# Optimization experiments

Hardware: AMD Instinct MI355X
Metric: run time of the kernel (lower is better)

The kernel has to match this reference:

```python
import jax, jax.numpy as jnp
import numpy as np

B, Nq, Nk, R = 4, 1024, 1024, 256
NH, DK, DV = 8, 64, 64


def setup_inputs() -> dict:
    key = jax.random.key(0)
    ks = jax.random.split(key, 16)
    mk = lambda k, shape, s=1.0: jax.random.normal(k, shape, dtype=jnp.float32) * s
    inp = {
        'Q_real': mk(ks[0], (B, Nq, R)), 'Q_imag': mk(ks[1], (B, Nq, R)),
        'K_real': mk(ks[2], (B, Nk, R)), 'K_imag': mk(ks[3], (B, Nk, R)),
        'V_real': mk(ks[4], (B, Nk, R)), 'V_imag': mk(ks[5], (B, Nk, R)),
        'WQ_r': mk(ks[6], (NH * DK, R), 0.02), 'WQ_i': mk(ks[7], (NH * DK, R), 0.02),
        'WK_r': mk(ks[8], (NH * DK, R), 0.02), 'WK_i': mk(ks[9], (NH * DK, R), 0.02),
        'WV_r': mk(ks[10], (NH * DV, R), 0.02), 'WV_i': mk(ks[11], (NH * DV, R), 0.02),
        'WO_r': mk(ks[12], (R, NH * DV), 0.02), 'WO_i': mk(ks[13], (R, NH * DV), 0.02),
        'mask': jax.random.randint(ks[14], (B, Nk), 0, 2).astype(bool),
    }
    return inp


def _complex_linear(x, w_r, w_i):
    # x: complex [..., in]; weights real [out, in]. Same math as 4 real matmuls.
    w = (w_r + 1j * w_i).astype(jnp.complex64)
    return x @ w.T


def reference(Q_real, Q_imag, K_real, K_imag, V_real, V_imag,
              WQ_r, WQ_i, WK_r, WK_i, WV_r, WV_i, WO_r, WO_i, mask):
    Q = (Q_real + 1j * Q_imag).astype(jnp.complex64)
    K = (K_real + 1j * K_imag).astype(jnp.complex64)
    V = (V_real + 1j * V_imag).astype(jnp.complex64)

    Qp = _complex_linear(Q, WQ_r, WQ_i).reshape(B, Nq, NH, DK).transpose(0, 2, 1, 3)
    Kp = _complex_linear(K, WK_r, WK_i).reshape(B, Nk, NH, DK).transpose(0, 2, 1, 3)
    Vp = _complex_linear(V, WV_r, WV_i).reshape(B, Nk, NH, DV).transpose(0, 2, 1, 3)

    # complex scores [B, NH, Nq, Nk]; conj on K matches torch .conj().transpose
    scores = jnp.einsum('bhqd,bhkd->bhqk', Qp, jnp.conj(Kp)) / jnp.sqrt(jnp.float32(DK))
    scores_abs = jnp.abs(scores)

    m = mask[:, None, None, :]                    # [B,1,1,Nk]
    valid = jnp.any(mask, axis=-1)[:, None, None, None]  # [B,1,1,1] valid query rows
    masked = jnp.where(m, scores_abs, -jnp.inf)
    # avoid all -inf rows feeding softmax (those rows are zeroed afterwards)
    safe = jnp.where(valid, masked, 0.0)
    w = jax.nn.softmax(safe, axis=-1)
    w = jnp.where(valid, w, 0.0)

    attn = jnp.einsum('bhqk,bhkd->bhqd', w.astype(Vp.dtype), Vp)
    attn = attn.transpose(0, 2, 1, 3).reshape(B, Nq, NH * DV)
    return _complex_linear(attn, WO_r, WO_i)
```

## Files before the change

kernel.cpp:

```cpp
#include <hip/hip_runtime.h>
#include <hip/hip_bf16.h>
#include <math.h>

#define NBATCH 4
#define NSEQ   1024
#define RD     256
#define NHEAD  8
#define HD     64
#define NHD    512

typedef __attribute__((ext_vector_type(8))) short  short8;
typedef __attribute__((ext_vector_type(4))) short  short4v;
typedef __attribute__((ext_vector_type(4))) float  float4v;

#define MFMA16(a,b,c) __builtin_amdgcn_mfma_f32_16x16x32_bf16(a,b,c,0,0,0)

typedef const void __attribute__((address_space(1)))* gas_t;
typedef void __attribute__((address_space(3)))* las_t;
#define GLOAD16(g, l) __builtin_amdgcn_global_load_lds((gas_t)(g), (las_t)(l), 16, 0, 0)

static __device__ __forceinline__ short f2b(float f) {
    __hip_bfloat16 h = __float2bfloat16(f);
    union { __hip_bfloat16 h; short s; } u; u.h = h;
    return u.s;
}
static __device__ __forceinline__ void st4(short* dst, float4v v) {
    short4v p;
    p[0] = f2b(v[0]); p[1] = f2b(v[1]);
    p[2] = f2b(v[2]); p[3] = f2b(v[3]);
    *(short4v*)dst = p;
}

struct ConvArgs { const float* src[15]; short* dst[15]; int n4[15]; };

__global__ __launch_bounds__(256) void convert_bf16(ConvArgs ca)
{
    const int a = blockIdx.y;
    if (a == 14) {
        if (blockIdx.x != 0) return;
        __shared__ int isByteLayout;
        const int t = threadIdx.x;
        if (t == 0) isByteLayout = 0;
        __syncthreads();
        const int* mi = (const int*)ca.src[14];
        #pragma unroll
        for (int j = 0; j < 4; j++) {
            int v = mi[t*4 + j];
            if (v & ~1) isByteLayout = 1;
        }
        __syncthreads();
        const unsigned char* mb = (const unsigned char*)ca.src[14];
        unsigned char mv[16];
        int lc = 0;
        if (isByteLayout) {
            #pragma unroll
            for (int j = 0; j < 16; j++) { mv[j] = mb[t*16 + j] ? 1 : 0; lc += mv[j]; }
        } else {
            #pragma unroll
            for (int j = 0; j < 16; j++) { mv[j] = mi[t*16 + j] ? 1 : 0; lc += mv[j]; }
        }
        const int lane = t & 63, b = t >> 6;
        int sum = lc;
        #pragma unroll
        for (int d = 1; d < 64; d <<= 1) {
            int o = __shfl_up(sum, d, 64);
            if (lane >= d) sum += o;
        }
        int p = sum - lc;
        unsigned short* idxOut = (unsigned short*)ca.dst[14];
        int* cntOut = (int*)(idxOut + 4096);
        unsigned short* ib = idxOut + b*1024;
        #pragma unroll
        for (int j = 0; j < 16; j++)
            if (mv[j]) ib[p++] = (unsigned short)(lane*16 + j);
        if (lane == 63) cntOut[b] = sum;
        return;
    }
    if (a >= 2 && a <= 5) {
        const int t = threadIdx.x;
        const int r0 = blockIdx.x * 16;
        const int b  = r0 >> 10;
        __shared__ int isByteLayout;
        __shared__ unsigned short ib[1024];
        __shared__ int scnt;
        if (t == 0) isByteLayout = 0;
        __syncthreads();
        const int* mi = (const int*)ca.src[14];
        #pragma unroll
        for (int j = 0; j < 4; j++) {
            int v = mi[t*4 + j];
            if (v & ~1) isByteLayout = 1;
        }
        __syncthreads();
        if (t < 64) {
            const unsigned char* mb8 = (const unsigned char*)ca.src[14];
            unsigned char mv[16]; int lc = 0;
            if (isByteLayout) {
                #pragma unroll
                for (int j = 0; j < 16; j++) { mv[j] = mb8[b*1024 + t*16 + j] ? 1 : 0; lc += mv[j]; }
            } else {
                #pragma unroll
                for (int j = 0; j < 16; j++) { mv[j] = mi[b*1024 + t*16 + j] ? 1 : 0; lc += mv[j]; }
            }
            int sum = lc;
            #pragma unroll
            for (int d = 1; d < 64; d <<= 1) {
                int o = __shfl_up(sum, d, 64);
                if (t >= d) sum += o;
            }
            int p = sum - lc;
            #pragma unroll
            for (int j = 0; j < 16; j++)
                if (mv[j]) ib[p++] = (unsigned short)(t*16 + j);
            if (t == 63) scnt = sum;
        }
        __syncthreads();
        const int cb = scnt, L = (cb + 63) & ~63;
        const float* __restrict__ s = ca.src[a];
        short* __restrict__ d = ca.dst[a];
        const int jj = t >> 4, c = t & 15;
        const int j  = r0 + jj;
        const int jl = j & 1023;
        if (jl < L) {
            short* dp = d + (size_t)j*RD + c*4;
            if (jl < cb) {
                const float* sp = s + ((size_t)(b*NSEQ) + ib[jl])*RD + c*4;
                #pragma unroll
                for (int u = 0; u < 4; u++) {
                    float4v v = *(const float4v*)(sp + u*64);
                    st4(dp + u*64, v);
                }
            } else {
                short4v z = {0,0,0,0};
                #pragma unroll
                for (int u = 0; u < 4; u++) *(short4v*)(dp + u*64) = z;
            }
        }
        return;
    }
    const float* __restrict__ s = ca.src[a];
    short* __restrict__ d = ca.dst[a];
    const int n4 = ca.n4[a];
    for (int i = blockIdx.x*256 + threadIdx.x; i < n4; i += gridDim.x*256) {
        float4v v = *(const float4v*)(s + (size_t)i*4);
        st4(d + (size_t)i*4, v);
    }
}

struct ProjArgs {
    const short* Xr[3]; const short* Xi[3];
    const short* Wr[3]; const short* Wi[3];
    short* Yr[3]; short* Yi[3];
    const int* cnt;
};

__global__ __launch_bounds__(256) void cgemm_proj(ProjArgs pa)
{
    __shared__ short sX[2][128][64];
    __shared__ short sW[2][64][64];
    const int z = blockIdx.z;
    const int n0 = blockIdx.x * 64, m0 = blockIdx.y * 128;
    if (z >= 1) {
        int b  = m0 >> 10;
        int nb = m0 & 1023;
        int L  = (pa.cnt[b] + 63) & ~63;
        if (nb >= L) return;
    }
    const short* __restrict__ X_r = pa.Xr[z];
    const short* __restrict__ X_i = pa.Xi[z];
    const short* __restrict__ W_r = pa.Wr[z];
    const short* __restrict__ W_i = pa.Wi[z];
    short* __restrict__ Y_r = pa.Yr[z];
    short* __restrict__ Y_i = pa.Yi[z];
    const int transposeOut = (z == 2);

    const int tid  = threadIdx.x;
    const int lane = tid & 63, wave = tid >> 6;
    const int quad = lane >> 4, l16 = lane & 15;
    const int sw8  = l16 & 7;
    const int rsub = lane >> 3;
    const int colg = (lane & 7) ^ rsub;

    const short nk = (short)0x8000;
    const short8 neg = {nk,nk,nk,nk,nk,nk,nk,nk};

    float4v zf = {0.f,0.f,0.f,0.f};
    float4v Yr[2][4], Yi[2][4];
    #pragma unroll
    for (int ms = 0; ms < 2; ms++)
        #pragma unroll
        for (int t = 0; t < 4; t++) { Yr[ms][t] = zf; Yi[ms][t] = zf; }

    for (int kc = 0; kc < RD; kc += 64) {
        __syncthreads();
        if (wave < 2) {
            const short* gp = wave ? X_i : X_r;
            short* lp = wave ? &sX[1][0][0] : &sX[0][0][0];
            #pragma unroll
            for (int j = 0; j < 16; j++) {
                int row = j*8 + rsub;
                GLOAD16(gp + (size_t)(m0 + row)*RD + kc + colg*8, lp + j*512);
            }
        } else {
            const short* gp = (wave == 3) ? W_i : W_r;
            short* lp = (wave == 3) ? &sW[1][0][0] : &sW[0][0][0];
            #pragma unroll
            for (int j = 0; j < 8; j++) {
                int row = j*8 + rsub;
                GLOAD16(gp + (size_t)(n0 + row)*RD + kc + colg*8, lp + j*512);
            }
        }
        __syncthreads();
        short8 fxr[2][2], fxi[2][2], fxin[2][2];
        #pragma unroll
        for (int ms = 0; ms < 2; ms++)
            #pragma unroll
            for (int ds = 0; ds < 2; ds++) {
                int row = wave*32 + ms*16 + l16;
                int u = ((ds*4 + quad) ^ sw8) * 8;
                fxr[ms][ds]  = *(short8*)&sX[0][row][u];
                fxi[ms][ds]  = *(short8*)&sX[1][row][u];
                fxin[ms][ds] = fxi[ms][ds] ^ neg;
            }
        #pragma unroll
        for (int t = 0; t < 4; t++)
            #pragma unroll
            for (int ds = 0; ds < 2; ds++) {
                int u = ((ds*4 + quad) ^ sw8) * 8;
                short8 wr = *(short8*)&sW[0][t*16 + l16][u];
                short8 wi = *(short8*)&sW[1][t*16 + l16][u];
                #pragma unroll
                for (int ms = 0; ms < 2; ms++) {
                    Yr[ms][t] = MFMA16(fxr[ms][ds],  wr, Yr[ms][t]);
                    Yr[ms][t] = MFMA16(fxin[ms][ds], wi, Yr[ms][t]);
                    Yi[ms][t] = MFMA16(fxr[ms][ds],  wi, Yi[ms][t]);
                    Yi[ms][t] = MFMA16(fxi[ms][ds],  wr, Yi[ms][t]);
                }
            }
    }

    const int b = m0 >> 10, h = n0 >> 6, nb = m0 & 1023;
    short* sT = &sX[0][0][0];
    short* Yp[2] = { Y_r, Y_i };
    #pragma unroll
    for (int p = 0; p < 2; p++) {
        __syncthreads();
        #pragma unroll
        for (int ms = 0; ms < 2; ms++)
            #pragma unroll
            for (int t = 0; t < 4; t++)
                #pragma unroll
                for (int r = 0; r < 4; r++) {
                    float v = p ? Yi[ms][t][r] : Yr[ms][t][r];
                    int rr = wave*32 + ms*16 + quad*4 + r;
                    int cc = t*16 + l16;
                    if (!transposeOut) sT[rr*68 + cc]  = f2b(v);
                    else               sT[cc*132 + rr] = f2b(v);
                }
        __syncthreads();
        #pragma unroll
        for (int it = 0; it < 4; it++) {
            int idx = it*256 + tid;
            int rr, c8;
            size_t o;
            const short* sp;
            if (!transposeOut) {
                rr = idx >> 3; c8 = (idx & 7)*8;
                sp = &sT[rr*68 + c8];
                o = (((size_t)(b*NHEAD + h))*NSEQ + nb + rr)*HD + c8;
            } else {
                rr = idx >> 4; c8 = (idx & 15)*8;
                sp = &sT[rr*132 + c8];
                o = (((size_t)(b*NHEAD + h))*HD + rr)*NSEQ + nb + c8;
            }
            short4v a = *(short4v*)sp;
            short4v bq = *(short4v*)(sp + 4);
            short8 v8 = { a[0],a[1],a[2],a[3], bq[0],bq[1],bq[2],bq[3] };
            *(short8*)&Yp[p][o] = v8;
        }
    }
}

__global__ __launch_bounds__(512) void attn_mfma(
    const short* __restrict__ Qp_r, const short* __restrict__ Qp_i,
    const short* __restrict__ Kp_r, const short* __restrict__ Kp_i,
    const short* __restrict__ Vp_r, const short* __restrict__ Vp_i,
    const int* __restrict__ cnt,
    short* __restrict__ Ar, short* __restrict__ Ai)
{
    __shared__ __align__(16) char smem[75776];
    short (*sP)[16][40] = (short(*)[16][40])(smem + 65536);

    const int tid  = threadIdx.x;
    const int lane = tid & 63, wave = tid >> 6;
    const int quad = lane >> 4, l16 = lane & 15;
    const int sw8  = l16 & 7;
    const int qstrip = wave >> 1;
    const int khalf  = wave & 1;
    const int qt = blockIdx.x >> 5;
    const int bh = blockIdx.x & 31;
    const int b  = bh >> 3, h = bh & 7;
    const size_t base = (size_t)bh * (NSEQ*HD);

    const int rsub = lane >> 3;
    const int colg = (lane & 7) ^ rsub;

    const int cb = cnt[b];
    const int nt = (cb + 63) >> 6;

    const int splane = wave >> 1;
    const short* sgp = (splane == 0) ? Kp_r : (splane == 1) ? Kp_i
                     : (splane == 2) ? Vp_r : Vp_i;
    const int sisV = (splane >= 2);
    const int soff = splane * 8192;

    const short nk = (short)0x8000;
    const short8 neg = {nk,nk,nk,nk,nk,nk,nk,nk};
    short8 fqr[2], fqi[2], fqrn[2];
    #pragma unroll
    for (int ds = 0; ds < 2; ds++) {
        size_t qo = base + (size_t)(qt*64 + qstrip*16 + l16)*HD + ds*32 + quad*8;
        fqr[ds]  = *(const short8*)&Qp_r[qo];
        fqi[ds]  = *(const short8*)&Qp_i[qo];
        fqrn[ds] = fqr[ds] ^ neg;
    }

    float4v zf = {0.f,0.f,0.f,0.f};
    float4v Or[4], Oi[4];
    float lrow[4];
    #pragma unroll
    for (int t = 0; t < 4; t++) { Or[t] = zf; Oi[t] = zf; }
    #pragma unroll
    for (int r = 0; r < 4; r++) lrow[r] = 0.f;

    const float C2 = 0.18033688f;

    if (nt > 0) {
        short* lp = (short*)(smem + soff);
        #pragma unroll
        for (int jj = 0; jj < 4; jj++) {
            int j = (wave & 1)*4 + jj;
            int row = j*8 + rsub;
            const short* g = sisV
                ? sgp + base + (size_t)row*NSEQ + colg*8
                : sgp + base + (size_t)row*HD + colg*8;
            GLOAD16(g, lp + j*512);
        }
    }

    for (int kt = 0; kt < nt; kt++) {
        __syncthreads();

        if (kt + 1 < nt) {
            const int kn = (kt + 1) * 64;
            short* lp = (short*)(smem + ((kt + 1) & 1)*32768 + soff);
            #pragma unroll
            for (int jj = 0; jj < 4; jj++) {
                int j = (wave & 1)*4 + jj;
                int row = j*8 + rsub;
                const short* g = sisV
                    ? sgp + base + (size_t)row*NSEQ + kn + colg*8
                    : sgp + base + (size_t)(kn + row)*HD + colg*8;
                GLOAD16(g, lp + j*512);
            }
        }

        const char* buf = smem + (kt & 1)*32768;
        short (*sK0)[64] = (short(*)[64])(buf);
        short (*sK1)[64] = (short(*)[64])(buf + 8192);
        short (*sV0)[64] = (short(*)[64])(buf + 16384);
        short (*sV1)[64] = (short(*)[64])(buf + 24576);
        const int k0 = kt*64;

        float4v Sr[2], Si[2];
        Sr[0] = zf; Sr[1] = zf; Si[0] = zf; Si[1] = zf;
        #pragma unroll
        for (int t = 0; t < 2; t++)
            #pragma unroll
            for (int ds = 0; ds < 2; ds++) {
                int u = ((ds*4 + quad) ^ sw8) * 8;
                int krow = khalf*32 + t*16 + l16;
                short8 kr = *(short8*)&sK0[krow][u];
                short8 ki = *(short8*)&sK1[krow][u];
                Sr[t] = MFMA16(fqr[ds],  kr, Sr[t]);
                Sr[t] = MFMA16(fqi[ds],  ki, Sr[t]);
                Si[t] = MFMA16(fqi[ds],  kr, Si[t]);
                Si[t] = MFMA16(fqrn[ds], ki, Si[t]);
            }

        #pragma unroll
        for (int t = 0; t < 2; t++) {
            bool mv = (k0 + khalf*32 + t*16 + l16) < cb;
            #pragma unroll
            for (int r = 0; r < 4; r++) {
                float a = Sr[t][r], c = Si[t][r];
                float x = fmaf(a, a, c*c);
                float s = __builtin_amdgcn_sqrtf(x);
                float e = mv ? __builtin_amdgcn_exp2f(C2 * s) : 0.f;
                lrow[r] += e;
                sP[wave][quad*4 + r][t*16 + l16] = f2b(e);
            }
        }

        {
            short8 fp = *(short8*)&sP[wave][l16][quad*8];
            #pragma unroll
            for (int t = 0; t < 4; t++) {
                int u = ((khalf*4 + quad) ^ sw8) * 8;
                short8 vr = *(short8*)&sV0[t*16 + l16][u];
                short8 vi = *(short8*)&sV1[t*16 + l16][u];
                Or[t] = MFMA16(fp, vr, Or[t]);
                Oi[t] = MFMA16(fp, vi, Oi[t]);
            }
        }
    }

    __syncthreads();
    float* sC = (float*)smem;
    float* sL = (float*)(smem + 32768);
    if (khalf == 1) {
        #pragma unroll
        for (int t = 0; t < 4; t++)
            #pragma unroll
            for (int r = 0; r < 4; r++) {
                int o8 = ((qstrip*4 + t)*64 + lane)*8 + r*2;
                sC[o8]     = Or[t][r];
                sC[o8 + 1] = Oi[t][r];
            }
        int lo = (qstrip*64 + lane)*4;
        #pragma unroll
        for (int r = 0; r < 4; r++) sL[lo + r] = lrow[r];
    }
    __syncthreads();
    if (khalf == 0) {
        #pragma unroll
        for (int t = 0; t < 4; t++)
            #pragma unroll
            for (int r = 0; r < 4; r++) {
                int o8 = ((qstrip*4 + t)*64 + lane)*8 + r*2;
                Or[t][r] += sC[o8];
                Oi[t][r] += sC[o8 + 1];
            }
        int lo = (qstrip*64 + lane)*4;
        float inv[4];
        #pragma unroll
        for (int r = 0; r < 4; r++) {
            float ls = lrow[r] + sL[lo + r];
            ls += __shfl_xor(ls, 1, 64);
            ls += __shfl_xor(ls, 2, 64);
            ls += __shfl_xor(ls, 4, 64);
            ls += __shfl_xor(ls, 8, 64);
            inv[r] = (ls > 0.f) ? 1.f/ls : 0.f;
        }
        #pragma unroll
        for (int t = 0; t < 4; t++)
            #pragma unroll
            for (int r = 0; r < 4; r++) {
                int q = qt*64 + qstrip*16 + quad*4 + r;
                int d = t*16 + l16;
                size_t o = ((size_t)(b*NSEQ + q))*NHD + h*HD + d;
                Ar[o] = f2b(Or[t][r] * inv[r]);
                Ai[o] = f2b(Oi[t][r] * inv[r]);
            }
    }
}

__global__ __launch_bounds__(256) void cgemm_out(
    const short* __restrict__ A_r, const short* __restrict__ A_i,
    const short* __restrict__ W_r, const short* __restrict__ W_i,
    float* __restrict__ Out, int writeImagPlane)
{
    __shared__ short sA[2][64][64];
    __shared__ short sW[2][32][64];
    const int tid  = threadIdx.x;
    const int lane = tid & 63, wave = tid >> 6;
    const int quad = lane >> 4, l16 = lane & 15;
    const int sw8  = l16 & 7;
    const int rsub = lane >> 3;
    const int colg = (lane & 7) ^ rsub;
    const int n0 = blockIdx.x * 32, m0 = blockIdx.y * 64;

    const short nk = (short)0x8000;
    const short8 neg = {nk,nk,nk,nk,nk,nk,nk,nk};

    float4v zf = {0.f,0.f,0.f,0.f};
    float4v Yr[2], Yi[2];
    #pragma unroll
    for (int t = 0; t < 2; t++) { Yr[t] = zf; Yi[t] = zf; }

    for (int kc = 0; kc < NHD; kc += 64) {
        __syncthreads();
        {
            if (wave < 2) {
                const short* gp = wave ? A_i : A_r;
                short* lp = wave ? &sA[1][0][0] : &sA[0][0][0];
                #pragma unroll
                for (int j = 0; j < 8; j++) {
                    int row = j*8 + rsub;
                    GLOAD16(gp + (size_t)(m0 + row)*NHD + kc + colg*8, lp + j*512);
                }
            } else {
                const short* gp = (wave == 3) ? W_i : W_r;
                short* lp = (wave == 3) ? &sW[1][0][0] : &sW[0][0][0];
                #pragma unroll
                for (int j = 0; j < 4; j++) {
                    int row = j*8 + rsub;
                    GLOAD16(gp + (size_t)(n0 + row)*NHD + kc + colg*8, lp + j*512);
                }
            }
        }
        __syncthreads();
        short8 far[2], fai[2], fain[2];
        #pragma unroll
        for (int ds = 0; ds < 2; ds++) {
            int u = ((ds*4 + quad) ^ sw8) * 8;
            far[ds]  = *(short8*)&sA[0][wave*16 + l16][u];
            fai[ds]  = *(short8*)&sA[1][wave*16 + l16][u];
            fain[ds] = fai[ds] ^ neg;
        }
        #pragma unroll
        for (int t = 0; t < 2; t++)
            #pragma unroll
            for (int ds = 0; ds < 2; ds++) {
                int u = ((ds*4 + quad) ^ sw8) * 8;
                short8 wr = *(short8*)&sW[0][t*16 + l16][u];
                short8 wi = *(short8*)&sW[1][t*16 + l16][u];
                Yr[t] = MFMA16(far[ds],  wr, Yr[t]);
                Yr[t] = MFMA16(fain[ds], wi, Yr[t]);
                Yi[t] = MFMA16(far[ds],  wi, Yi[t]);
                Yi[t] = MFMA16(fai[ds],  wr, Yi[t]);
            }
    }
    const size_t TOT = (size_t)NBATCH * NSEQ * RD;
    #pragma unroll
    for (int t = 0; t < 2; t++)
        #pragma unroll
        for (int r = 0; r < 4; r++) {
            int row = m0 + wave*16 + quad*4 + r;
            int col = n0 + t*16 + l16;
            size_t o = (size_t)row*RD + col;
            Out[o] = Yr[t][r];
            if (writeImagPlane) Out[o + TOT] = Yi[t][r];
        }
}

extern "C" void kernel_launch(void* const* d_in, const int* in_sizes, int n_in,
                              void* d_out, int out_size, void* d_ws, size_t ws_size,
                              hipStream_t stream)
{
    float* out = (float*)d_out;

    const size_t P = (size_t)NBATCH * NHEAD * NSEQ * HD;
    const size_t H = (size_t)NBATCH * NSEQ * RD;
    const size_t WSZ = (size_t)NHD * RD;

    short* bws = (short*)d_ws;
    short* Qpr = bws + 0*P;  short* Qpi = bws + 1*P;
    short* Kpr = bws + 2*P;  short* Kpi = bws + 3*P;
    short* Vpr = bws + 4*P;  short* Vpi = bws + 5*P;
    short* conv = bws + 6*P;
    short* cX[6]; for (int i = 0; i < 6; i++) cX[i] = conv + i*H;
    short* cW[6]; for (int i = 0; i < 6; i++) cW[i] = conv + 6*H + i*WSZ;
    short* cWOr = conv + 6*H + 6*WSZ;
    short* cWOi = conv + 6*H + 7*WSZ;
    unsigned short* midx = (unsigned short*)(conv + 6*H + 8*WSZ);
    int* mcnt = (int*)(midx + 4096);
    short* Apr = conv;
    short* Api = conv + P;

    const size_t TOT = (size_t)NBATCH * NSEQ * RD;
    const int writeImagPlane = ((size_t)out_size >= 2*TOT) ? 1 : 0;

    ConvArgs ca;
    for (int i = 0; i < 6; i++) {
        ca.src[i] = (const float*)d_in[i];  ca.dst[i] = cX[i];  ca.n4[i] = (int)(H/4);
    }
    for (int i = 0; i < 6; i++) {
        ca.src[6+i] = (const float*)d_in[6+i]; ca.dst[6+i] = cW[i]; ca.n4[6+i] = (int)(WSZ/4);
    }
    ca.src[12] = (const float*)d_in[12]; ca.dst[12] = cWOr; ca.n4[12] = (int)(WSZ/4);
    ca.src[13] = (const float*)d_in[13]; ca.dst[13] = cWOi; ca.n4[13] = (int)(WSZ/4);
    ca.src[14] = (const float*)d_in[14]; ca.dst[14] = (short*)midx; ca.n4[14] = 0;

    ProjArgs pa;
    pa.Xr[0] = cX[0]; pa.Xi[0] = cX[1];
    pa.Xr[1] = cX[2]; pa.Xi[1] = cX[3];
    pa.Xr[2] = cX[4]; pa.Xi[2] = cX[5];
    pa.Wr[0] = cW[0]; pa.Wi[0] = cW[1];
    pa.Wr[1] = cW[2]; pa.Wi[1] = cW[3];
    pa.Wr[2] = cW[4]; pa.Wi[2] = cW[5];
    pa.Yr[0] = Qpr; pa.Yi[0] = Qpi;
    pa.Yr[1] = Kpr; pa.Yi[1] = Kpi;
    pa.Yr[2] = Vpr; pa.Yi[2] = Vpi;
    pa.cnt = mcnt;

    convert_bf16<<<dim3(256, 15), 256, 0, stream>>>(ca);
    cgemm_proj<<<dim3(8, 32, 3), 256, 0, stream>>>(pa);
    attn_mfma<<<dim3(512), 512, 0, stream>>>(Qpr, Qpi, Kpr, Kpi, Vpr, Vpi,
                                             mcnt, Apr, Api);
    cgemm_out<<<dim3(8, 64), 256, 0, stream>>>(Apr, Api, cWOr, cWOi, out,
                                               writeImagPlane);
}
```

Baseline: 158.8 us.

## Double-buffer LDS tiles in projection and output complex GEMMs

Both the QKV projection GEMM and the output GEMM now keep two LDS stages and issue the async global-to-LDS loads for the next K chunk before computing on the current one, with a single barrier per iteration. The projection kernel also narrows its K chunk to 32 and uses a matching 4-way XOR swizzle so the doubled buffers fit in the same LDS footprint. This is meant to hide global load latency behind MFMA work, at the cost of more iterations in the projection and twice the LDS in the output kernel, which may lower occupancy.

```diff
diff --git a/kernel.cpp b/kernel.cpp
--- a/kernel.cpp
+++ b/kernel.cpp
@@ -1,6 +1,5 @@
 #include <hip/hip_runtime.h>
 #include <hip/hip_bf16.h>
-#include <math.h>
 
 #define NBATCH 4
 #define NSEQ   1024
@@ -156,8 +155,8 @@
 
 __global__ __launch_bounds__(256) void cgemm_proj(ProjArgs pa)
 {
-    __shared__ short sX[2][128][64];
-    __shared__ short sW[2][64][64];
+    __shared__ short sX[2][2][128][32];
+    __shared__ short sW[2][2][64][32];
     const int z = blockIdx.z;
     const int n0 = blockIdx.x * 64, m0 = blockIdx.y * 128;
     if (z >= 1) {
@@ -177,9 +176,8 @@
     const int tid  = threadIdx.x;
     const int lane = tid & 63, wave = tid >> 6;
     const int quad = lane >> 4, l16 = lane & 15;
-    const int sw8  = l16 & 7;
-    const int rsub = lane >> 3;
-    const int colg = (lane & 7) ^ rsub;
+    const int lrow = lane >> 2;
+    const int scg  = (lane & 3) ^ (lrow & 3);
 
     const short nk = (short)0x8000;
     const short8 neg = {nk,nk,nk,nk,nk,nk,nk,nk};
@@ -191,56 +189,57 @@
         #pragma unroll
         for (int t = 0; t < 4; t++) { Yr[ms][t] = zf; Yi[ms][t] = zf; }
 
-    for (int kc = 0; kc < RD; kc += 64) {
-        __syncthreads();
-        if (wave < 2) {
-            const short* gp = wave ? X_i : X_r;
-            short* lp = wave ? &sX[1][0][0] : &sX[0][0][0];
-            #pragma unroll
-            for (int j = 0; j < 16; j++) {
-                int row = j*8 + rsub;
-                GLOAD16(gp + (size_t)(m0 + row)*RD + kc + colg*8, lp + j*512);
-            }
-        } else {
-            const short* gp = (wave == 3) ? W_i : W_r;
-            short* lp = (wave == 3) ? &sW[1][0][0] : &sW[0][0][0];
-            #pragma unroll
-            for (int j = 0; j < 8; j++) {
-                int row = j*8 + rsub;
-                GLOAD16(gp + (size_t)(n0 + row)*RD + kc + colg*8, lp + j*512);
-            }
-        }
-        __syncthreads();
-        short8 fxr[2][2], fxi[2][2], fxin[2][2];
-        #pragma unroll
-        for (int ms = 0; ms < 2; ms++)
-            #pragma unroll
-            for (int ds = 0; ds < 2; ds++) {
-                int row = wave*32 + ms*16 + l16;
-                int u = ((ds*4 + quad) ^ sw8) * 8;
-                fxr[ms][ds]  = *(short8*)&sX[0][row][u];
-                fxi[ms][ds]  = *(short8*)&sX[1][row][u];
-                fxin[ms][ds] = fxi[ms][ds] ^ neg;
-            }
-        #pragma unroll
-        for (int t = 0; t < 4; t++)
-            #pragma unroll
-            for (int ds = 0; ds < 2; ds++) {
-                int u = ((ds*4 + quad) ^ sw8) * 8;
-                short8 wr = *(short8*)&sW[0][t*16 + l16][u];
-                short8 wi = *(short8*)&sW[1][t*16 + l16][u];
-                #pragma unroll
-                for (int ms = 0; ms < 2; ms++) {
-                    Yr[ms][t] = MFMA16(fxr[ms][ds],  wr, Yr[ms][t]);
-                    Yr[ms][t] = MFMA16(fxin[ms][ds], wi, Yr[ms][t]);
-                    Yi[ms][t] = MFMA16(fxr[ms][ds],  wi, Yi[ms][t]);
-                    Yi[ms][t] = MFMA16(fxi[ms][ds],  wr, Yi[ms][t]);
-                }
-            }
-    }
+    #define PROJ_STAGE(kc, bf)                                                \
+        if (wave < 2) {                                                       \
+            const short* gp = wave ? X_i : X_r;                               \
+            short* lp = &sX[bf][wave][0][0];                                  \
+            _Pragma("unroll")                                                 \
+            for (int j = 0; j < 8; j++)                                       \
+                GLOAD16(gp + (size_t)(m0 + j*16 + lrow)*RD + (kc) + scg*8,    \
+                        lp + j*512);                                          \
+        } else {                                                              \
+            const short* gp = (wave == 3) ? W_i : W_r;                        \
+            short* lp = &sW[bf][wave - 2][0][0];                              \
+            _Pragma("unroll")                                                 \
+            for (int j = 0; j < 4; j++)                                       \
+                GLOAD16(gp + (size_t)(n0 + j*16 + lrow)*RD + (kc) + scg*8,    \
+                        lp + j*512);                                          \
+        }
+
+    PROJ_STAGE(0, 0);
+
+    const int xsh = l16 & 3;
+    for (int c = 0; c < 8; c++) {
+        __syncthreads();
+        if (c + 1 < 8) { PROJ_STAGE((c + 1)*32, (c + 1) & 1); }
+        const int bf = c & 1;
+        const int u = (quad ^ xsh) * 8;
+
+        short8 fxr[2], fxi[2], fxin[2];
+        #pragma unroll
+        for (int ms = 0; ms < 2; ms++) {
+            int row = wave*32 + ms*16 + l16;
+            fxr[ms]  = *(short8*)&sX[bf][0][row][u];
+            fxi[ms]  = *(short8*)&sX[bf][1][row][u];
+            fxin[ms] = fxi[ms] ^ neg;
+        }
+        #pragma unroll
+        for (int t = 0; t < 4; t++) {
+            short8 wr = *(short8*)&sW[bf][0][t*16 + l16][u];
+            short8 wi = *(short8*)&sW[bf][1][t*16 + l16][u];
+            #pragma unroll
+            for (int ms = 0; ms < 2; ms++) {
+                Yr[ms][t] = MFMA16(fxr[ms],  wr, Yr[ms][t]);
+                Yr[ms][t] = MFMA16(fxin[ms], wi, Yr[ms][t]);
+                Yi[ms][t] = MFMA16(fxr[ms],  wi, Yi[ms][t]);
+                Yi[ms][t] = MFMA16(fxi[ms],  wr, Yi[ms][t]);
+            }
+        }
+    }
+    #undef PROJ_STAGE
 
     const int b = m0 >> 10, h = n0 >> 6, nb = m0 & 1023;
-    short* sT = &sX[0][0][0];
+    short* sT = &sX[0][0][0][0];
     short* Yp[2] = { Y_r, Y_i };
     #pragma unroll
     for (int p = 0; p < 2; p++) {
@@ -470,8 +469,8 @@
     const short* __restrict__ W_r, const short* __restrict__ W_i,
     float* __restrict__ Out, int writeImagPlane)
 {
-    __shared__ short sA[2][64][64];
-    __shared__ short sW[2][32][64];
+    __shared__ short sA[2][2][64][64];
+    __shared__ short sW[2][2][32][64];
     const int tid  = threadIdx.x;
     const int lane = tid & 63, wave = tid >> 6;
     const int quad = lane >> 4, l16 = lane & 15;
@@ -488,34 +487,36 @@
     #pragma unroll
     for (int t = 0; t < 2; t++) { Yr[t] = zf; Yi[t] = zf; }
 
-    for (int kc = 0; kc < NHD; kc += 64) {
-        __syncthreads();
-        {
-            if (wave < 2) {
-                const short* gp = wave ? A_i : A_r;
-                short* lp = wave ? &sA[1][0][0] : &sA[0][0][0];
-                #pragma unroll
-                for (int j = 0; j < 8; j++) {
-                    int row = j*8 + rsub;
-                    GLOAD16(gp + (size_t)(m0 + row)*NHD + kc + colg*8, lp + j*512);
-                }
-            } else {
-                const short* gp = (wave == 3) ? W_i : W_r;
-                short* lp = (wave == 3) ? &sW[1][0][0] : &sW[0][0][0];
-                #pragma unroll
-                for (int j = 0; j < 4; j++) {
-                    int row = j*8 + rsub;
-                    GLOAD16(gp + (size_t)(n0 + row)*NHD + kc + colg*8, lp + j*512);
-                }
-            }
-        }
-        __syncthreads();
+    #define OUT_STAGE(kc, bf)                                                 \
+        if (wave < 2) {                                                       \
+            const short* gp = wave ? A_i : A_r;                               \
+            short* lp = &sA[bf][wave][0][0];                                  \
+            _Pragma("unroll")                                                 \
+            for (int j = 0; j < 8; j++)                                       \
+                GLOAD16(gp + (size_t)(m0 + j*8 + rsub)*NHD + (kc) + colg*8,   \
+                        lp + j*512);                                          \
+        } else {                                                              \
+            const short* gp = (wave == 3) ? W_i : W_r;                        \
+            short* lp = &sW[bf][wave - 2][0][0];                              \
+            _Pragma("unroll")                                                 \
+            for (int j = 0; j < 4; j++)                                       \
+                GLOAD16(gp + (size_t)(n0 + j*8 + rsub)*NHD + (kc) + colg*8,   \
+                        lp + j*512);                                          \
+        }
+
+    OUT_STAGE(0, 0);
+
+    for (int c = 0; c < 8; c++) {
+        __syncthreads();
+        if (c + 1 < 8) { OUT_STAGE((c + 1)*64, (c + 1) & 1); }
+        const int bf = c & 1;
+
         short8 far[2], fai[2], fain[2];
         #pragma unroll
         for (int ds = 0; ds < 2; ds++) {
             int u = ((ds*4 + quad) ^ sw8) * 8;
-            far[ds]  = *(short8*)&sA[0][wave*16 + l16][u];
-            fai[ds]  = *(short8*)&sA[1][wave*16 + l16][u];
+            far[ds]  = *(short8*)&sA[bf][0][wave*16 + l16][u];
+            fai[ds]  = *(short8*)&sA[bf][1][wave*16 + l16][u];
             fain[ds] = fai[ds] ^ neg;
         }
         #pragma unroll
@@ -523,14 +524,16 @@
             #pragma unroll
             for (int ds = 0; ds < 2; ds++) {
                 int u = ((ds*4 + quad) ^ sw8) * 8;
-                short8 wr = *(short8*)&sW[0][t*16 + l16][u];
-                short8 wi = *(short8*)&sW[1][t*16 + l16][u];
+                short8 wr = *(short8*)&sW[bf][0][t*16 + l16][u];
+                short8 wi = *(short8*)&sW[bf][1][t*16 + l16][u];
                 Yr[t] = MFMA16(far[ds],  wr, Yr[t]);
                 Yr[t] = MFMA16(fain[ds], wi, Yr[t]);
                 Yi[t] = MFMA16(far[ds],  wi, Yi[t]);
                 Yi[t] = MFMA16(fai[ds],  wr, Yi[t]);
             }
     }
+    #undef OUT_STAGE
+
     const size_t TOT = (size_t)NBATCH * NSEQ * RD;
     #pragma unroll
     for (int t = 0; t < 2; t++)
```

Result: faster. 152.4 us (-4.0%).
